# Performance work log

Hardware: AMD Instinct MI355X
Metric: run time of the kernel (lower is better)

## Reference

```python
import jax, jax.numpy as jnp
import numpy as np

ETA = 1e-5  # option['eta']


def setup_inputs() -> dict:
    key = jax.random.key(0)
    k1, k2, k3, k4 = jax.random.split(key, 4)
    d, N, two_m = 1024, 20000, 512  # num_feature, num_data, 2*m
    At = jax.random.normal(k1, (d, N), dtype=jnp.float32)
    b = jax.random.normal(k2, (N,), dtype=jnp.float32)
    w1_init = jax.random.normal(k3, (d,), dtype=jnp.float32)
    W2_init = jax.random.normal(k4, (two_m, d - 1), dtype=jnp.float32)
    return {"At": At, "b": b, "w1_init": w1_init, "W2_init": W2_init}


def _ftrl_scan(At, b, w1_init, W2_init):
    # Sequential FTRL-style online FM update (task='reg'), faithful to the torch loop.
    def step(carry, xs):
        w1, W2, g_w1, g_W2 = carry
        x, bi = xs                     # x: (d,), bi: scalar
        a = x[:-1]                     # alpha[:-1], (d-1,)
        t = W2 @ a                     # (2m,) == W2.matmul(alpha[:-1])
        scalar = jnp.dot(w1, x) + jnp.dot(t, t)   # w1^T x + t^T t
        sign = 2.0 * (scalar - bi)     # grad of squared loss
        g_w1 = g_w1 + sign * x
        g_W2 = g_W2 + 2.0 * jnp.outer(t, a)       # 2 * (W2 a) a^T
        w1_new = -ETA * g_w1
        W2_new = -ETA * g_W2
        return (w1_new, W2_new, g_w1, g_W2), scalar

    carry0 = (w1_init, W2_init, jnp.zeros_like(w1_init), jnp.zeros_like(W2_init))
    _, preds = jax.lax.scan(step, carry0, (At.T, b))  # scan over num_data
    return preds


def reference(At, b, w1_init, W2_init):
    preds = _ftrl_scan(At, b, w1_init, W2_init)
    return preds, b  # (pred_list, real_list)
```

## Files before the change

### kernel.cpp

```cpp
#include <hip/hip_runtime.h>


#define NN 20000
#define CC 8
#define NCH 2500
#define ETA2 2e-5f
#define XST 1032

#define OFF_GRAM 0L
#define OFF_Z    70016L
#define OFF_SCLP 2630016L
#define OFF_ACC  2630080L
#define OFF_TV   2650112L
#define OFF_X0   2670144L
#define OFF_XC   2671168L
#define WS_NEED_BYTES ((size_t)(OFF_XC + 20480000L) * 4)

__global__ __launch_bounds__(1024) void k_init(
    const float* __restrict__ At, const float* __restrict__ bvec,
    const float* __restrict__ w1, const float* __restrict__ W2,
    float* __restrict__ out, float* __restrict__ scalp,
    float* __restrict__ x0ws) {
  __shared__ float x0s[1024];
  __shared__ float part[16];
  const int bid = blockIdx.x, t = threadIdx.x;
  const int wid = t >> 6, lane = t & 63;

  if (bid < 32) {
    x0s[t] = (t < 1023) ? At[(long)t * NN] : 0.f;
    __syncthreads();
    const int row = bid * 16 + wid;
    float p = 0.f;
#pragma unroll
    for (int k = 0; k < 16; ++k) {
      const int ci = k * 64 + lane;
      if (ci < 1023) p = fmaf(W2[(long)row * 1023 + ci], x0s[ci], p);
    }
#pragma unroll
    for (int o = 32; o > 0; o >>= 1) p += __shfl_down(p, o);
    if (lane == 0) part[wid] = p * p;
    __syncthreads();
    if (t == 0) {
      float s = 0.f;
#pragma unroll
      for (int k = 0; k < 16; ++k) s += part[k];
      scalp[bid] = s;
    }
  } else if (bid == 32) {
    const float xv = At[(long)t * NN];
    x0ws[t] = xv;
    float p = w1[t] * xv;
#pragma unroll
    for (int o = 32; o > 0; o >>= 1) p += __shfl_down(p, o);
    if (lane == 0) part[wid] = p;
    __syncthreads();
    if (t == 0) {
      float s = 0.f;
#pragma unroll
      for (int k = 0; k < 16; ++k) s += part[k];
      scalp[32] = s;
    }
  } else {
    const int i = (bid - 33) * 1000 + t;
    if (t < 1000) out[NN + i] = bvec[i];
  }
}

#define STAGE8(g, xl)                                               \
  {                                                                 \
    const int e_ = (g) >> 1, q_ = (g) & 1;                          \
    const float4 v_ =                                               \
        *(const float4*)(At + (long)e_ * NN + i0 + 4 * q_);         \
    xl[(4 * q_ + 0) * XST + e_] = v_.x;                             \
    xl[(4 * q_ + 1) * XST + e_] = v_.y;                             \
    xl[(4 * q_ + 2) * XST + e_] = v_.z;                             \
    xl[(4 * q_ + 3) * XST + e_] = v_.w;                             \
  }

struct GramSh {
  __align__(16) float xl[CC * XST];
  __align__(16) float x0s[1024];
  float usum[CC];
  float rs[CC];
  float sc[2];
};
static_assert(sizeof(GramSh) <= 64 * 1024, "LDS must stay under 64KB");

__global__ __launch_bounds__(1024, 4) void k_gram(
    const float* __restrict__ At, const float* __restrict__ bvec,
    const float* __restrict__ x0g, float* __restrict__ gram,
    float* __restrict__ Zr, const float* __restrict__ scalp,
    float* __restrict__ acc, float* __restrict__ Xc, const int writeXc) {
  __shared__ GramSh sh;
  const int c = blockIdx.x, t = threadIdx.x;
  const long i0 = (long)c * CC;

  sh.x0s[t] = x0g[t];
  if (t == 0) {
    float T = 0.f;
#pragma unroll
    for (int k = 0; k < 32; ++k) T += scalp[k];
    sh.sc[0] = T;
    sh.sc[1] = scalp[32];
  }

  STAGE8(t, sh.xl);
  STAGE8(1024 + t, sh.xl);
  __syncthreads();

  if (t < 896) {
    const int pi = t >> 5, band = t & 31;
    int i = 1;
    while ((i + 1) * i / 2 <= pi) ++i;
    const int j = pi - i * (i - 1) / 2;
    float p = 0.f;
#pragma unroll
    for (int k = 0; k < 8; ++k) {
      const int ef = (band + 32 * k) * 4;
      const float4 A = *(const float4*)&sh.xl[i * XST + ef];
      const float4 B = *(const float4*)&sh.xl[j * XST + ef];
      p = fmaf(A.x, B.x, p);
      p = fmaf(A.y, B.y, p);
      p = fmaf(A.z, B.z, p);
      p = fmaf(A.w, B.w, p);
    }
#pragma unroll
    for (int off = 16; off >= 1; off >>= 1) p += __shfl_xor(p, off);
    if (band == 0) gram[(long)c * 28 + pi] = p;
  } else {
    const int uz = t - 896, uj = uz >> 4, b16 = uz & 15;
    float p = 0.f;
#pragma unroll
    for (int k = 0; k < 16; ++k) {
      const int ef = (b16 + 16 * k) * 4;
      const float4 X = *(const float4*)&sh.xl[uj * XST + ef];
      const float4 X0 = *(const float4*)&sh.x0s[ef];
      p = fmaf(X.x, X0.x, p);
      p = fmaf(X.y, X0.y, p);
      p = fmaf(X.z, X0.z, p);
      p = fmaf(X.w, X0.w, p);
    }
#pragma unroll
    for (int off = 8; off >= 1; off >>= 1) p += __shfl_xor(p, off);
    if (b16 == 0) sh.usum[uj] = p;
  }
  __syncthreads();

  if (t < CC) {
    const long gi = i0 + t;
    const float uu = sh.usum[t];
    const float qi = sh.xl[t * XST + 1023];
    const float q0 = sh.x0s[1023];
    const float al = (gi == 0) ? 1.f : -ETA2 * (uu - q0 * qi);
    const float T0 = sh.sc[0], s0v = sh.sc[1];
    const float bv = bvec[gi];
    float r = 2.f * fmaf(al * al, T0, -bv);
    if (gi == 0) r = 2.f * (s0v + T0 - bv);
    sh.rs[t] = r;
    acc[gi] = r;
  }
  __syncthreads();

  {
    float x[CC];
#pragma unroll
    for (int j = 0; j < CC; ++j) x[j] = sh.xl[j * XST + t];
    float z = 0.f;
#pragma unroll
    for (int j = 0; j < CC; ++j) z = fmaf(sh.rs[j], x[j], z);
    Zr[(long)c * 1024 + t] = z;
    if (writeXc) {
      float* dst = Xc + ((long)c * 1024 + t) * CC;
      *(float4*)dst = make_float4(x[0], x[1], x[2], x[3]);
      *(float4*)(dst + 4) = make_float4(x[4], x[5], x[6], x[7]);
    }
  }
}

__global__ __launch_bounds__(1024) void k_scan(float* __restrict__ Z) {
  __shared__ float gsum[32][33];
  const int t = threadIdx.x;
  const int ei = t & 31, ci = t >> 5;
  const int e = blockIdx.x * 32 + ei;
  const int c0 = ci * 79;
  const int c1 = (c0 + 79 < NCH) ? c0 + 79 : NCH;

  float s = 0.f;
  for (int base = c0; base < c1; base += 8) {
    float v[8];
#pragma unroll
    for (int k = 0; k < 8; ++k) {
      const int cc = base + k;
      v[k] = (cc < c1) ? Z[(long)cc * 1024 + e] : 0.f;
    }
#pragma unroll
    for (int k = 0; k < 8; ++k) s += v[k];
  }
  gsum[ci][ei] = s;
  __syncthreads();

  float off = 0.f;
#pragma unroll
  for (int k = 0; k < 31; ++k)
    if (k < ci) off += gsum[k][ei];

  s = off;
  for (int base = c0; base < c1; base += 8) {
    float v[8];
#pragma unroll
    for (int k = 0; k < 8; ++k) {
      const int cc = base + k;
      v[k] = (cc < c1) ? Z[(long)cc * 1024 + e] : 0.f;
    }
#pragma unroll
    for (int k = 0; k < 8; ++k) {
      const int cc = base + k;
      if (cc < c1) Z[(long)cc * 1024 + e] = s;
      s += v[k];
    }
  }
}

template <bool TR, bool LAST>
__global__ __launch_bounds__(1024, 4) void k_term(
    const float* __restrict__ At, const float* __restrict__ bvec,
    const float* __restrict__ gram, const float* __restrict__ S,
    float* __restrict__ Z1, float* __restrict__ acc, float* __restrict__ tvec,
    float* __restrict__ out, const float* __restrict__ Xc) {
  __shared__ float red[16][CC];
  __shared__ float vvs[CC], wvs[CC];
  __shared__ float xl[TR ? 16 : CC * XST];
  const int c = blockIdx.x, t = threadIdx.x;
  const int wid = t >> 6, lane = t & 63;
  const long i0 = (long)c * CC;

  if (t < CC) vvs[t] = LAST ? tvec[i0 + t] : acc[i0 + t];

  float x[CC];
  if (TR) {
    const float* src = Xc + ((long)c * 1024 + t) * CC;
    const float4 a = *(const float4*)src;
    const float4 b4 = *(const float4*)(src + 4);
    x[0] = a.x; x[1] = a.y; x[2] = a.z; x[3] = a.w;
    x[4] = b4.x; x[5] = b4.y; x[6] = b4.z; x[7] = b4.w;
  } else {
    STAGE8(t, xl);
    STAGE8(1024 + t, xl);
    __syncthreads();
#pragma unroll
    for (int j = 0; j < CC; ++j) x[j] = xl[j * XST + t];
  }

  const float sv = S[(long)c * 1024 + t];
  float p[CC];
#pragma unroll
  for (int j = 0; j < CC; ++j) p[j] = x[j] * sv;
#pragma unroll
  for (int off = 32; off >= 1; off >>= 1)
#pragma unroll
    for (int j = 0; j < CC; ++j) p[j] += __shfl_xor(p[j], off);
  if (lane == 0)
#pragma unroll
    for (int j = 0; j < CC; ++j) red[wid][j] = p[j];
  __syncthreads();

  if (t < CC) {
    const int i = t;
    float dot = 0.f;
#pragma unroll
    for (int k = 0; k < 16; ++k) dot += red[k][i];
    const float* grow = gram + (long)c * 28 + i * (i - 1) / 2;
    float g = 0.f;
#pragma unroll
    for (int j = 0; j < CC - 1; ++j)
      if (j < i) g = fmaf(grow[j], vvs[j], g);
    const float w = -ETA2 * (dot + g);
    if (LAST) {
      out[i0 + i] = fmaf(0.5f, acc[i0 + i] + w, bvec[i0 + i]);
    } else {
      wvs[i] = w;
      tvec[i0 + i] = w;
      acc[i0 + i] += w;
    }
  }
  if (!LAST) {
    __syncthreads();
    float z = 0.f;
#pragma unroll
    for (int j = 0; j < CC; ++j) z = fmaf(wvs[j], x[j], z);
    Z1[(long)c * 1024 + t] = z;
  }
}

extern "C" void kernel_launch(void* const* d_in, const int* in_sizes, int n_in,
                              void* d_out, int out_size, void* d_ws,
                              size_t ws_size, hipStream_t stream) {
  const float* At = (const float*)d_in[0];
  const float* b  = (const float*)d_in[1];
  const float* w1 = (const float*)d_in[2];
  const float* W2 = (const float*)d_in[3];
  float* out = (float*)d_out;
  float* ws = (float*)d_ws;

  float* gram  = ws + OFF_GRAM;
  float* Zsh   = ws + OFF_Z;
  float* scalp = ws + OFF_SCLP;
  float* acc   = ws + OFF_ACC;
  float* tvec  = ws + OFF_TV;
  float* x0ws  = ws + OFF_X0;
  float* Xc    = ws + OFF_XC;

  const int bigws = (ws_size >= WS_NEED_BYTES) ? 1 : 0;

  k_init<<<dim3(53), dim3(1024), 0, stream>>>(At, b, w1, W2, out, scalp, x0ws);
  k_gram<<<dim3(NCH), dim3(1024), 0, stream>>>(At, b, x0ws, gram, Zsh, scalp,
                                               acc, Xc, bigws);
  k_scan<<<dim3(32), dim3(1024), 0, stream>>>(Zsh);
  if (bigws) {
    k_term<true, false><<<dim3(NCH), dim3(1024), 0, stream>>>(
        At, b, gram, Zsh, Zsh, acc, tvec, out, Xc);
    k_scan<<<dim3(32), dim3(1024), 0, stream>>>(Zsh);
    k_term<true, true><<<dim3(NCH), dim3(1024), 0, stream>>>(
        At, b, gram, Zsh, Zsh, acc, tvec, out, Xc);
  } else {
    k_term<false, false><<<dim3(NCH), dim3(1024), 0, stream>>>(
        At, b, gram, Zsh, Zsh, acc, tvec, out, Xc);
    k_scan<<<dim3(32), dim3(1024), 0, stream>>>(Zsh);
    k_term<false, true><<<dim3(NCH), dim3(1024), 0, stream>>>(
        At, b, gram, Zsh, Zsh, acc, tvec, out, Xc);
  }
}
```

Before: 253.2 us.

## Double chunk size to 16 rows and compute Gram via 4x4 register tiles

Chunk size grows from 8 to 16 data rows, halving the block count and the Z buffer size that the scan kernels traverse. The Gram matrix is now computed with 4x4 register-blocked wave tiles over an unpadded LDS layout, and the x0 dot product reads x0 straight from global memory. The transposed Xc copy is removed, so the term kernels re-stage At from global memory instead. This trades extra At reads and a 64KB LDS footprint, which lowers occupancy, for less Z traffic and fewer launches' worth of blocks.

```diff
diff --git a/kernel.cpp b/kernel.cpp
--- a/kernel.cpp
+++ b/kernel.cpp
@@ -2,19 +2,16 @@
 
 
 #define NN 20000
-#define CC 8
-#define NCH 2500
+#define CC 16
+#define NCH 1250
 #define ETA2 2e-5f
-#define XST 1032
 
 #define OFF_GRAM 0L
-#define OFF_Z    70016L
-#define OFF_SCLP 2630016L
-#define OFF_ACC  2630080L
-#define OFF_TV   2650112L
-#define OFF_X0   2670144L
-#define OFF_XC   2671168L
-#define WS_NEED_BYTES ((size_t)(OFF_XC + 20480000L) * 4)
+#define OFF_Z    150016L
+#define OFF_SCLP 1430016L
+#define OFF_ACC  1430080L
+#define OFF_TV   1450080L
+#define OFF_X0   1470080L
 
 __global__ __launch_bounds__(1024) void k_init(
     const float* __restrict__ At, const float* __restrict__ bvec,
@@ -66,115 +63,127 @@
   }
 }
 
-#define STAGE8(g, xl)                                               \
-  {                                                                 \
-    const int e_ = (g) >> 1, q_ = (g) & 1;                          \
-    const float4 v_ =                                               \
-        *(const float4*)(At + (long)e_ * NN + i0 + 4 * q_);         \
-    xl[(4 * q_ + 0) * XST + e_] = v_.x;                             \
-    xl[(4 * q_ + 1) * XST + e_] = v_.y;                             \
-    xl[(4 * q_ + 2) * XST + e_] = v_.z;                             \
-    xl[(4 * q_ + 3) * XST + e_] = v_.w;                             \
-  }
-
-struct GramSh {
-  __align__(16) float xl[CC * XST];
-  __align__(16) float x0s[1024];
-  float usum[CC];
-  float rs[CC];
-  float sc[2];
-};
-static_assert(sizeof(GramSh) <= 64 * 1024, "LDS must stay under 64KB");
+#define STAGE16(g)                                                      \
+  {                                                                     \
+    const int e_ = (g) >> 2, q_ = (g) & 3;                              \
+    const float4 v_ =                                                   \
+        *(const float4*)(At + (long)e_ * NN + i0 + 4 * q_);             \
+    xl[((4 * q_ + 0) << 10) | e_] = v_.x;                               \
+    xl[((4 * q_ + 1) << 10) | e_] = v_.y;                               \
+    xl[((4 * q_ + 2) << 10) | e_] = v_.z;                               \
+    xl[((4 * q_ + 3) << 10) | e_] = v_.w;                               \
+  }
 
 __global__ __launch_bounds__(1024, 4) void k_gram(
     const float* __restrict__ At, const float* __restrict__ bvec,
     const float* __restrict__ x0g, float* __restrict__ gram,
     float* __restrict__ Zr, const float* __restrict__ scalp,
-    float* __restrict__ acc, float* __restrict__ Xc, const int writeXc) {
-  __shared__ GramSh sh;
+    float* __restrict__ acc) {
+  __shared__ float xl[16384];
   const int c = blockIdx.x, t = threadIdx.x;
   const long i0 = (long)c * CC;
-
-  sh.x0s[t] = x0g[t];
-  if (t == 0) {
-    float T = 0.f;
-#pragma unroll
-    for (int k = 0; k < 32; ++k) T += scalp[k];
-    sh.sc[0] = T;
-    sh.sc[1] = scalp[32];
-  }
-
-  STAGE8(t, sh.xl);
-  STAGE8(1024 + t, sh.xl);
-  __syncthreads();
-
-  if (t < 896) {
-    const int pi = t >> 5, band = t & 31;
-    int i = 1;
-    while ((i + 1) * i / 2 <= pi) ++i;
-    const int j = pi - i * (i - 1) / 2;
+  const int wv = t >> 6, lane = t & 63;
+
+  STAGE16(t);
+  STAGE16(1024 + t);
+  STAGE16(2048 + t);
+  STAGE16(3072 + t);
+  __syncthreads();
+
+  float r_val = 0.f;
+  bool is_alpha = false;
+
+  if (wv < 10) {
+    int a = 0, rr = wv;
+    while (rr > a) { rr -= ++a; }
+    const int bb = rr;
+    float ac[16];
+#pragma unroll
+    for (int k = 0; k < 16; ++k) ac[k] = 0.f;
+#pragma unroll
+    for (int k = 0; k < 4; ++k) {
+      const int f4 = 4 * (lane + 64 * k);
+      const float4 A0 = *(const float4*)&xl[((4 * a + 0) << 10) | f4];
+      const float4 A1 = *(const float4*)&xl[((4 * a + 1) << 10) | f4];
+      const float4 A2 = *(const float4*)&xl[((4 * a + 2) << 10) | f4];
+      const float4 A3 = *(const float4*)&xl[((4 * a + 3) << 10) | f4];
+      const float4 B0 = *(const float4*)&xl[((4 * bb + 0) << 10) | f4];
+      const float4 B1 = *(const float4*)&xl[((4 * bb + 1) << 10) | f4];
+      const float4 B2 = *(const float4*)&xl[((4 * bb + 2) << 10) | f4];
+      const float4 B3 = *(const float4*)&xl[((4 * bb + 3) << 10) | f4];
+      const float4 RA[4] = {A0, A1, A2, A3};
+      const float4 RB[4] = {B0, B1, B2, B3};
+#pragma unroll
+      for (int r_ = 0; r_ < 4; ++r_)
+#pragma unroll
+        for (int s_ = 0; s_ < 4; ++s_) {
+          ac[r_ * 4 + s_] = fmaf(RA[r_].x, RB[s_].x, ac[r_ * 4 + s_]);
+          ac[r_ * 4 + s_] = fmaf(RA[r_].y, RB[s_].y, ac[r_ * 4 + s_]);
+          ac[r_ * 4 + s_] = fmaf(RA[r_].z, RB[s_].z, ac[r_ * 4 + s_]);
+          ac[r_ * 4 + s_] = fmaf(RA[r_].w, RB[s_].w, ac[r_ * 4 + s_]);
+        }
+    }
+#pragma unroll
+    for (int off = 32; off >= 1; off >>= 1)
+#pragma unroll
+      for (int k = 0; k < 16; ++k) ac[k] += __shfl_xor(ac[k], off);
+    if (lane == 0) {
+      float* gp = gram + (long)c * 120;
+#pragma unroll
+      for (int r_ = 0; r_ < 4; ++r_) {
+        const int row = 4 * a + r_;
+        const int base = row * (row - 1) / 2;
+#pragma unroll
+        for (int s_ = 0; s_ < 4; ++s_) {
+          const int col = 4 * bb + s_;
+          if (col < row) gp[base + col] = ac[r_ * 4 + s_];
+        }
+      }
+    }
+  } else if (wv == 15) {
+    const int uj = lane & 15, ug = lane >> 4;
     float p = 0.f;
-#pragma unroll
-    for (int k = 0; k < 8; ++k) {
-      const int ef = (band + 32 * k) * 4;
-      const float4 A = *(const float4*)&sh.xl[i * XST + ef];
-      const float4 B = *(const float4*)&sh.xl[j * XST + ef];
-      p = fmaf(A.x, B.x, p);
-      p = fmaf(A.y, B.y, p);
-      p = fmaf(A.z, B.z, p);
-      p = fmaf(A.w, B.w, p);
-    }
-#pragma unroll
-    for (int off = 16; off >= 1; off >>= 1) p += __shfl_xor(p, off);
-    if (band == 0) gram[(long)c * 28 + pi] = p;
-  } else {
-    const int uz = t - 896, uj = uz >> 4, b16 = uz & 15;
-    float p = 0.f;
-#pragma unroll
-    for (int k = 0; k < 16; ++k) {
-      const int ef = (b16 + 16 * k) * 4;
-      const float4 X = *(const float4*)&sh.xl[uj * XST + ef];
-      const float4 X0 = *(const float4*)&sh.x0s[ef];
-      p = fmaf(X.x, X0.x, p);
-      p = fmaf(X.y, X0.y, p);
-      p = fmaf(X.z, X0.z, p);
-      p = fmaf(X.w, X0.w, p);
-    }
-#pragma unroll
-    for (int off = 8; off >= 1; off >>= 1) p += __shfl_xor(p, off);
-    if (b16 == 0) sh.usum[uj] = p;
-  }
-  __syncthreads();
-
-  if (t < CC) {
-    const long gi = i0 + t;
-    const float uu = sh.usum[t];
-    const float qi = sh.xl[t * XST + 1023];
-    const float q0 = sh.x0s[1023];
-    const float al = (gi == 0) ? 1.f : -ETA2 * (uu - q0 * qi);
-    const float T0 = sh.sc[0], s0v = sh.sc[1];
-    const float bv = bvec[gi];
-    float r = 2.f * fmaf(al * al, T0, -bv);
-    if (gi == 0) r = 2.f * (s0v + T0 - bv);
-    sh.rs[t] = r;
-    acc[gi] = r;
-  }
-  __syncthreads();
-
-  {
-    float x[CC];
-#pragma unroll
-    for (int j = 0; j < CC; ++j) x[j] = sh.xl[j * XST + t];
-    float z = 0.f;
-#pragma unroll
-    for (int j = 0; j < CC; ++j) z = fmaf(sh.rs[j], x[j], z);
-    Zr[(long)c * 1024 + t] = z;
-    if (writeXc) {
-      float* dst = Xc + ((long)c * 1024 + t) * CC;
-      *(float4*)dst = make_float4(x[0], x[1], x[2], x[3]);
-      *(float4*)(dst + 4) = make_float4(x[4], x[5], x[6], x[7]);
-    }
-  }
+#pragma unroll 8
+    for (int k = 0; k < 64; ++k) {
+      const int f = ug * 64 + ((k + uj) & 63);
+      const float4 xv = *(const float4*)&xl[(uj << 10) | (4 * f)];
+      const float4 x0 = *(const float4*)(x0g + 4 * f);
+      p = fmaf(xv.x, x0.x, p);
+      p = fmaf(xv.y, x0.y, p);
+      p = fmaf(xv.z, x0.z, p);
+      p = fmaf(xv.w, x0.w, p);
+    }
+    p += __shfl_xor(p, 16);
+    p += __shfl_xor(p, 32);
+    if (lane < 16) {
+      const long gi = i0 + lane;
+      const float qi = xl[(lane << 10) | 1023];
+      const float q0 = x0g[1023];
+      float T0 = 0.f;
+#pragma unroll
+      for (int k = 0; k < 32; ++k) T0 += scalp[k];
+      const float s0v = scalp[32];
+      const float bv = bvec[gi];
+      const float al = (gi == 0) ? 1.f : -ETA2 * (p - q0 * qi);
+      r_val = 2.f * fmaf(al * al, T0, -bv);
+      if (gi == 0) r_val = 2.f * (s0v + T0 - bv);
+      acc[gi] = r_val;
+      is_alpha = true;
+    }
+  }
+
+  float x[16];
+#pragma unroll
+  for (int j = 0; j < 16; ++j) x[j] = xl[(j << 10) | t];
+  __syncthreads();
+
+  if (is_alpha) xl[lane] = r_val;
+  __syncthreads();
+
+  float z = 0.f;
+#pragma unroll
+  for (int j = 0; j < 16; ++j) z = fmaf(xl[j], x[j], z);
+  Zr[(long)c * 1024 + t] = z;
 }
 
 __global__ __launch_bounds__(1024) void k_scan(float* __restrict__ Z) {
@@ -182,8 +191,8 @@
   const int t = threadIdx.x;
   const int ei = t & 31, ci = t >> 5;
   const int e = blockIdx.x * 32 + ei;
-  const int c0 = ci * 79;
-  const int c1 = (c0 + 79 < NCH) ? c0 + 79 : NCH;
+  const int c0 = ci * 40;
+  const int c1 = (c0 + 40 < NCH) ? c0 + 40 : NCH;
 
   float s = 0.f;
   for (int base = c0; base < c1; base += 8) {
@@ -221,73 +230,69 @@
   }
 }
 
-template <bool TR, bool LAST>
+template <bool LAST>
 __global__ __launch_bounds__(1024, 4) void k_term(
     const float* __restrict__ At, const float* __restrict__ bvec,
     const float* __restrict__ gram, const float* __restrict__ S,
     float* __restrict__ Z1, float* __restrict__ acc, float* __restrict__ tvec,
-    float* __restrict__ out, const float* __restrict__ Xc) {
-  __shared__ float red[16][CC];
-  __shared__ float vvs[CC], wvs[CC];
-  __shared__ float xl[TR ? 16 : CC * XST];
+    float* __restrict__ out) {
+  __shared__ float xl[16384];
   const int c = blockIdx.x, t = threadIdx.x;
-  const int wid = t >> 6, lane = t & 63;
   const long i0 = (long)c * CC;
-
-  if (t < CC) vvs[t] = LAST ? tvec[i0 + t] : acc[i0 + t];
-
-  float x[CC];
-  if (TR) {
-    const float* src = Xc + ((long)c * 1024 + t) * CC;
-    const float4 a = *(const float4*)src;
-    const float4 b4 = *(const float4*)(src + 4);
-    x[0] = a.x; x[1] = a.y; x[2] = a.z; x[3] = a.w;
-    x[4] = b4.x; x[5] = b4.y; x[6] = b4.z; x[7] = b4.w;
-  } else {
-    STAGE8(t, xl);
-    STAGE8(1024 + t, xl);
-    __syncthreads();
-#pragma unroll
-    for (int j = 0; j < CC; ++j) x[j] = xl[j * XST + t];
-  }
+  const int wv = t >> 6, lane = t & 63;
 
   const float sv = S[(long)c * 1024 + t];
-  float p[CC];
-#pragma unroll
-  for (int j = 0; j < CC; ++j) p[j] = x[j] * sv;
-#pragma unroll
-  for (int off = 32; off >= 1; off >>= 1)
-#pragma unroll
-    for (int j = 0; j < CC; ++j) p[j] += __shfl_xor(p[j], off);
-  if (lane == 0)
-#pragma unroll
-    for (int j = 0; j < CC; ++j) red[wid][j] = p[j];
-  __syncthreads();
-
-  if (t < CC) {
+
+  STAGE16(t);
+  STAGE16(1024 + t);
+  STAGE16(2048 + t);
+  STAGE16(3072 + t);
+  __syncthreads();
+
+  float x[16];
+#pragma unroll
+  for (int j = 0; j < 16; ++j) x[j] = xl[(j << 10) | t];
+  __syncthreads();
+
+#pragma unroll
+  for (int h = 0; h < 2; ++h) {
+    float ph[8];
+#pragma unroll
+    for (int i = 0; i < 8; ++i) ph[i] = x[h * 8 + i] * sv;
+#pragma unroll
+    for (int off = 32; off >= 1; off >>= 1)
+#pragma unroll
+      for (int i = 0; i < 8; ++i) ph[i] += __shfl_xor(ph[i], off);
+    if (lane == 0)
+#pragma unroll
+      for (int i = 0; i < 8; ++i) xl[(h * 8 + i) * 16 + wv] = ph[i];
+  }
+  __syncthreads();
+
+  if (t < 16) {
     const int i = t;
     float dot = 0.f;
 #pragma unroll
-    for (int k = 0; k < 16; ++k) dot += red[k][i];
-    const float* grow = gram + (long)c * 28 + i * (i - 1) / 2;
+    for (int k = 0; k < 16; ++k) dot += xl[i * 16 + k];
+    const float* grow = gram + (long)c * 120 + i * (i - 1) / 2;
     float g = 0.f;
 #pragma unroll
-    for (int j = 0; j < CC - 1; ++j)
-      if (j < i) g = fmaf(grow[j], vvs[j], g);
+    for (int j = 0; j < 15; ++j)
+      if (j < i) g = fmaf(grow[j], LAST ? tvec[i0 + j] : acc[i0 + j], g);
     const float w = -ETA2 * (dot + g);
     if (LAST) {
       out[i0 + i] = fmaf(0.5f, acc[i0 + i] + w, bvec[i0 + i]);
     } else {
-      wvs[i] = w;
       tvec[i0 + i] = w;
       acc[i0 + i] += w;
+      xl[256 + i] = w;
     }
   }
   if (!LAST) {
     __syncthreads();
     float z = 0.f;
 #pragma unroll
-    for (int j = 0; j < CC; ++j) z = fmaf(wvs[j], x[j], z);
+    for (int j = 0; j < 16; ++j) z = fmaf(xl[256 + j], x[j], z);
     Z1[(long)c * 1024 + t] = z;
   }
 }
@@ -308,25 +313,14 @@
   float* acc   = ws + OFF_ACC;
   float* tvec  = ws + OFF_TV;
   float* x0ws  = ws + OFF_X0;
-  float* Xc    = ws + OFF_XC;
-
-  const int bigws = (ws_size >= WS_NEED_BYTES) ? 1 : 0;
 
   k_init<<<dim3(53), dim3(1024), 0, stream>>>(At, b, w1, W2, out, scalp, x0ws);
   k_gram<<<dim3(NCH), dim3(1024), 0, stream>>>(At, b, x0ws, gram, Zsh, scalp,
-                                               acc, Xc, bigws);
+                                               acc);
   k_scan<<<dim3(32), dim3(1024), 0, stream>>>(Zsh);
-  if (bigws) {
-    k_term<true, false><<<dim3(NCH), dim3(1024), 0, stream>>>(
-        At, b, gram, Zsh, Zsh, acc, tvec, out, Xc);
-    k_scan<<<dim3(32), dim3(1024), 0, stream>>>(Zsh);
-    k_term<true, true><<<dim3(NCH), dim3(1024), 0, stream>>>(
-        At, b, gram, Zsh, Zsh, acc, tvec, out, Xc);
-  } else {
-    k_term<false, false><<<dim3(NCH), dim3(1024), 0, stream>>>(
-        At, b, gram, Zsh, Zsh, acc, tvec, out, Xc);
-    k_scan<<<dim3(32), dim3(1024), 0, stream>>>(Zsh);
-    k_term<false, true><<<dim3(NCH), dim3(1024), 0, stream>>>(
-        At, b, gram, Zsh, Zsh, acc, tvec, out, Xc);
-  }
-}
+  k_term<false><<<dim3(NCH), dim3(1024), 0, stream>>>(At, b, gram, Zsh, Zsh,
+                                                      acc, tvec, out);
+  k_scan<<<dim3(32), dim3(1024), 0, stream>>>(Zsh);
+  k_term<true><<<dim3(NCH), dim3(1024), 0, stream>>>(At, b, gram, Zsh, Zsh,
+                                                     acc, tvec, out);
+}
```

Measured after the change: 233.3 us. 1.09x faster.
